# Performance work log

Hardware: AMD Instinct MI355X
Metric: run time of the kernel (lower is better)

The kernel has to match this reference:

```python
import jax, jax.numpy as jnp
import numpy as np

N = 4096        # nodes
E = 262144      # edges (avg degree 64)
F_IN = 8        # num_features
EMB = 4         # embedding_dim
HEADS = 4
G1 = 64         # GATConv1_dim (concat -> 256)
G2 = 16         # GATConv2_dim (concat -> d_model=64)
D = HEADS * G2  # 64
FF = 32         # ff_hid_dim
GRAPHS = 8
OUT = 4         # output_dim
SLOPE_GAT = 0.2   # PyG GATConv negative_slope
SLOPE = 0.01      # F.leaky_relu default

def _p(k, shape, scale=0.1):
    return jax.random.normal(k, shape, jnp.float32) * scale

def setup_inputs() -> dict:
    key = jax.random.key(0)
    ks = jax.random.split(key, 16)
    return {
        "x": jax.random.normal(ks[0], (N, F_IN), jnp.float32),
        "edge_index": jax.random.randint(ks[1], (2, E), 0, N),
        "batch": jnp.sort(jax.random.randint(ks[2], (N,), 0, GRAPHS)),
        "W_feat": _p(ks[3], (F_IN, EMB)), "b_feat": jnp.zeros((EMB,), jnp.float32),
        "W1": _p(ks[4], (EMB, HEADS * G1)), "as1": _p(ks[5], (HEADS, G1)), "ad1": _p(ks[6], (HEADS, G1)), "b1": jnp.zeros((HEADS * G1,), jnp.float32),
        "W2": _p(ks[7], (HEADS * G1, HEADS * G2)), "as2": _p(ks[8], (HEADS, G2)), "ad2": _p(ks[9], (HEADS, G2)), "b2": jnp.zeros((HEADS * G2,), jnp.float32),
        "enc_W1": _p(ks[10], (D, FF)), "enc_b1": jnp.zeros((FF,), jnp.float32),
        "enc_W2": _p(ks[11], (FF, D)), "enc_b2": jnp.zeros((D,), jnp.float32),
        "dec_W1": _p(ks[12], (D, FF)), "dec_b1": jnp.zeros((FF,), jnp.float32),
        "dec_W2": _p(ks[13], (FF, D)), "dec_b2": jnp.zeros((D,), jnp.float32),
        "W_fc": _p(ks[14], (D, OUT)), "b_fc": jnp.zeros((OUT,), jnp.float32),
    }

def _gat(x, src, dst, W, a_s, a_d, b, n):
    # PyG GATConv: h = W x; e_ij = LeakyReLU(a_src.h_j + a_dst.h_i); softmax over
    # edges grouped by destination i; out_i = sum_j alpha_ij h_j; concat heads + bias.
    h = (x @ W).reshape(n, HEADS, -1)                      # [N,H,C]
    logits = (h * a_s).sum(-1)[src] + (h * a_d).sum(-1)[dst]  # [E,H]
    e = jax.nn.leaky_relu(logits, SLOPE_GAT)
    m = jax.ops.segment_max(e, dst, num_segments=n)        # [N,H]
    ex = jnp.exp(e - m[dst])
    den = jax.ops.segment_sum(ex, dst, num_segments=n)
    alpha = ex / (den[dst] + 1e-16)                        # [E,H]
    out = jax.ops.segment_sum(h[src] * alpha[:, :, None], dst, num_segments=n)
    return out.reshape(n, -1) + b

def reference(x, edge_index, batch, W_feat, b_feat, W1, as1, ad1, b1, W2, as2, ad2, b2, enc_W1, enc_b1, enc_W2, enc_b2, dec_W1, dec_b1, dec_W2, dec_b2, W_fc, b_fc):
    src, dst = edge_index[0], edge_index[1]
    h = x @ W_feat + b_feat                                # feature_fc
    h = jax.nn.leaky_relu(_gat(h, src, dst, W1, as1, ad1, b1, N), SLOPE)
    h = jax.nn.leaky_relu(_gat(h, src, dst, W2, as2, ad2, b2, N), SLOPE)
    # Source bug preserved: encoder/decoder MultiheadAttention outputs are computed
    # and then DISCARDED (FFN reads the layer input), so attention never affects the
    # output and is omitted here (pure dead code). Encoder output `memory` is also
    # unused by the decoder FFN, but is computed for parity.
    memory = jax.nn.relu(jax.nn.relu(h @ enc_W1 + enc_b1) @ enc_W2 + enc_b2)
    t = jax.nn.relu(jax.nn.relu(h @ dec_W1 + dec_b1) @ dec_W2 + dec_b2)
    cnt = jax.ops.segment_sum(jnp.ones((N,), jnp.float32), batch, num_segments=GRAPHS)
    pooled = jax.ops.segment_sum(t, batch, num_segments=GRAPHS) / jnp.maximum(cnt, 1.0)[:, None]
    return pooled @ W_fc + b_fc                            # [GRAPHS, OUT]
```

## Files before the change

### kernel.cpp

```cpp
#include <hip/hip_runtime.h>
#include <math.h>

#define NN 4096
#define EE 262144
#define NCHUNK 64
#define CHSZ 4096
#define PAD 128
#define NGRAPHS 8

__device__ __forceinline__ float lrelu(float x, float s){ return x > 0.f ? x : s*x; }

__global__ __launch_bounds__(256) void k_n1hist(
    const float* __restrict__ x, const float* __restrict__ Wf,
    const float* __restrict__ bf, const float* __restrict__ W1,
    const float* __restrict__ as1, const float* __restrict__ ad1,
    const int* __restrict__ ei,
    float* __restrict__ emb4, float* __restrict__ asum1, float* __restrict__ adsum1,
    int* __restrict__ hist){
  __shared__ int shi[NN];
  int t = threadIdx.x, b = blockIdx.x;
  if (b < NCHUNK){
    for (int v=t; v<NN; v+=256) shi[v]=0;
    __syncthreads();
    int base = b*CHSZ;
    #pragma unroll
    for (int i=0;i<16;i++){
      int d = ei[EE + base + i*256 + t];
      atomicAdd(&shi[d], 1);
    }
    __syncthreads();
    for (int v=t; v<NN; v+=256) hist[b*NN + v] = shi[v];
    return;
  }
  int wid = t >> 6, lane = t & 63;
  int n = (b - NCHUNK)*4 + wid;
  float e0=bf[0], e1=bf[1], e2=bf[2], e3=bf[3];
  #pragma unroll
  for (int k=0;k<8;k++){
    float xv = x[n*8+k];
    e0 += xv*Wf[k*4+0]; e1 += xv*Wf[k*4+1];
    e2 += xv*Wf[k*4+2]; e3 += xv*Wf[k*4+3];
  }
  if (lane == 0) *(float4*)&emb4[n*4] = make_float4(e0,e1,e2,e3);
  int c0 = lane*4;
  float4 w0 = *(const float4*)&W1[0*256+c0];
  float4 w1 = *(const float4*)&W1[1*256+c0];
  float4 w2 = *(const float4*)&W1[2*256+c0];
  float4 w3 = *(const float4*)&W1[3*256+c0];
  float4 hv;
  hv.x = e0*w0.x + e1*w1.x + e2*w2.x + e3*w3.x;
  hv.y = e0*w0.y + e1*w1.y + e2*w2.y + e3*w3.y;
  hv.z = e0*w0.z + e1*w1.z + e2*w2.z + e3*w3.z;
  hv.w = e0*w0.w + e1*w1.w + e2*w2.w + e3*w3.w;
  int hh = lane>>4, idx = c0 & 63;
  float4 as = *(const float4*)&as1[hh*64+idx];
  float4 ad = *(const float4*)&ad1[hh*64+idx];
  float ps = hv.x*as.x + hv.y*as.y + hv.z*as.z + hv.w*as.w;
  float pd = hv.x*ad.x + hv.y*ad.y + hv.z*ad.z + hv.w*ad.w;
  #pragma unroll
  for (int m=1;m<16;m<<=1){ ps += __shfl_xor(ps,m,64); pd += __shfl_xor(pd,m,64); }
  if ((lane&15)==0){ asum1[n*4+hh]=ps; adsum1[n*4+hh]=pd; }
}

__global__ __launch_bounds__(256) void k_scatter(
    const int* __restrict__ ei, const int* __restrict__ hist,
    int* __restrict__ esrc, int* __restrict__ deg){
  __shared__ int shi[NN];
  int t = threadIdx.x, c = blockIdx.x;
  int acc[16];
  #pragma unroll
  for (int i=0;i<16;i++) acc[i]=0;
  for (int cp=0; cp<c; cp++){
    #pragma unroll
    for (int i=0;i<16;i++) acc[i] += hist[cp*NN + i*256 + t];
  }
  #pragma unroll
  for (int i=0;i<16;i++) shi[i*256+t] = (i*256+t)*PAD + acc[i];
  if (c == NCHUNK-1){
    #pragma unroll
    for (int i=0;i<16;i++) deg[i*256+t] = acc[i] + hist[c*NN + i*256 + t];
  }
  __syncthreads();
  int base = c*CHSZ;
  #pragma unroll
  for (int i=0;i<16;i++){
    int e = base + i*256 + t;
    int d = ei[EE+e], sr = ei[e];
    int pos = atomicAdd(&shi[d], 1);
    esrc[pos] = sr;
  }
}

__global__ __launch_bounds__(1024) void k_gat1n2(
    const int* __restrict__ deg, const int* __restrict__ esrc,
    const float* __restrict__ emb4, const float* __restrict__ asum1,
    const float* __restrict__ adsum1, const float* __restrict__ b1,
    const float* __restrict__ W1, const float* __restrict__ W2,
    const float* __restrict__ as2, const float* __restrict__ ad2,
    float* __restrict__ h2, float* __restrict__ asum2, float* __restrict__ adsum2){
  __shared__ __align__(16) float g1s[16*256];
  __shared__ __align__(16) float4 w2t[1024];
  int t = threadIdx.x, w = t>>6, lane = t&63;
  const int n = blockIdx.x*16 + w;
  const int start = n*PAD;
  const int dg = deg[n];
  const int hh = lane>>4;
  float4 adst = *(const float4*)&adsum1[n*4];
  int k0 = lane, k1 = lane+64;
  int j0 = esrc[start + (k0<dg ? k0 : 0)];
  int j1 = esrc[start + (k1<dg ? k1 : 0)];
  float4 a0 = *(const float4*)&asum1[j0*4];
  float4 a1 = *(const float4*)&asum1[j1*4];
  float4 mx;
  mx.x = k0<dg ? a0.x : -INFINITY;  mx.y = k0<dg ? a0.y : -INFINITY;
  mx.z = k0<dg ? a0.z : -INFINITY;  mx.w = k0<dg ? a0.w : -INFINITY;
  if (k1<dg){
    mx.x=fmaxf(mx.x,a1.x); mx.y=fmaxf(mx.y,a1.y);
    mx.z=fmaxf(mx.z,a1.z); mx.w=fmaxf(mx.w,a1.w);
  }
  #pragma unroll
  for (int m=1;m<64;m<<=1){
    mx.x=fmaxf(mx.x,__shfl_xor(mx.x,m,64));
    mx.y=fmaxf(mx.y,__shfl_xor(mx.y,m,64));
    mx.z=fmaxf(mx.z,__shfl_xor(mx.z,m,64));
    mx.w=fmaxf(mx.w,__shfl_xor(mx.w,m,64));
  }
  float4 mh;
  mh.x = lrelu(mx.x+adst.x,0.2f); mh.y = lrelu(mx.y+adst.y,0.2f);
  mh.z = lrelu(mx.z+adst.z,0.2f); mh.w = lrelu(mx.w+adst.w,0.2f);
  float4 ex0 = make_float4(0.f,0.f,0.f,0.f), ex1 = make_float4(0.f,0.f,0.f,0.f);
  if (k0<dg){
    ex0.x = expf(lrelu(a0.x+adst.x,0.2f)-mh.x);
    ex0.y = expf(lrelu(a0.y+adst.y,0.2f)-mh.y);
    ex0.z = expf(lrelu(a0.z+adst.z,0.2f)-mh.z);
    ex0.w = expf(lrelu(a0.w+adst.w,0.2f)-mh.w);
  }
  if (k1<dg){
    ex1.x = expf(lrelu(a1.x+adst.x,0.2f)-mh.x);
    ex1.y = expf(lrelu(a1.y+adst.y,0.2f)-mh.y);
    ex1.z = expf(lrelu(a1.z+adst.z,0.2f)-mh.z);
    ex1.w = expf(lrelu(a1.w+adst.w,0.2f)-mh.w);
  }
  float4 den = make_float4(ex0.x+ex1.x, ex0.y+ex1.y, ex0.z+ex1.z, ex0.w+ex1.w);
  #pragma unroll
  for (int m=1;m<64;m<<=1){
    den.x += __shfl_xor(den.x,m,64); den.y += __shfl_xor(den.y,m,64);
    den.z += __shfl_xor(den.z,m,64); den.w += __shfl_xor(den.w,m,64);
  }
  float4 al0, al1;
  al0.x = ex0.x/(den.x+1e-16f); al0.y = ex0.y/(den.y+1e-16f);
  al0.z = ex0.z/(den.z+1e-16f); al0.w = ex0.w/(den.w+1e-16f);
  al1.x = ex1.x/(den.x+1e-16f); al1.y = ex1.y/(den.y+1e-16f);
  al1.z = ex1.z/(den.z+1e-16f); al1.w = ex1.w/(den.w+1e-16f);
  float4 e0v = *(const float4*)&emb4[j0*4];
  float4 e1v = *(const float4*)&emb4[j1*4];
  float4 s0, s1, s2, s3;
  s0.x = al0.x*e0v.x + al1.x*e1v.x; s0.y = al0.x*e0v.y + al1.x*e1v.y;
  s0.z = al0.x*e0v.z + al1.x*e1v.z; s0.w = al0.x*e0v.w + al1.x*e1v.w;
  s1.x = al0.y*e0v.x + al1.y*e1v.x; s1.y = al0.y*e0v.y + al1.y*e1v.y;
  s1.z = al0.y*e0v.z + al1.y*e1v.z; s1.w = al0.y*e0v.w + al1.y*e1v.w;
  s2.x = al0.z*e0v.x + al1.z*e1v.x; s2.y = al0.z*e0v.y + al1.z*e1v.y;
  s2.z = al0.z*e0v.z + al1.z*e1v.z; s2.w = al0.z*e0v.w + al1.z*e1v.w;
  s3.x = al0.w*e0v.x + al1.w*e1v.x; s3.y = al0.w*e0v.y + al1.w*e1v.y;
  s3.z = al0.w*e0v.z + al1.w*e1v.z; s3.w = al0.w*e0v.w + al1.w*e1v.w;
  #pragma unroll
  for (int m=1;m<64;m<<=1){
    s0.x += __shfl_xor(s0.x,m,64); s0.y += __shfl_xor(s0.y,m,64);
    s0.z += __shfl_xor(s0.z,m,64); s0.w += __shfl_xor(s0.w,m,64);
    s1.x += __shfl_xor(s1.x,m,64); s1.y += __shfl_xor(s1.y,m,64);
    s1.z += __shfl_xor(s1.z,m,64); s1.w += __shfl_xor(s1.w,m,64);
    s2.x += __shfl_xor(s2.x,m,64); s2.y += __shfl_xor(s2.y,m,64);
    s2.z += __shfl_xor(s2.z,m,64); s2.w += __shfl_xor(s2.w,m,64);
    s3.x += __shfl_xor(s3.x,m,64); s3.y += __shfl_xor(s3.y,m,64);
    s3.z += __shfl_xor(s3.z,m,64); s3.w += __shfl_xor(s3.w,m,64);
  }
  float4 sh = (hh==0) ? s0 : (hh==1) ? s1 : (hh==2) ? s2 : s3;
  const int c0 = lane*4;
  float4 w0 = *(const float4*)&W1[0*256+c0];
  float4 w1 = *(const float4*)&W1[1*256+c0];
  float4 w2 = *(const float4*)&W1[2*256+c0];
  float4 w3 = *(const float4*)&W1[3*256+c0];
  float4 bb = *(const float4*)&b1[c0];
  float4 o;
  o.x = lrelu(sh.x*w0.x + sh.y*w1.x + sh.z*w2.x + sh.w*w3.x + bb.x, 0.01f);
  o.y = lrelu(sh.x*w0.y + sh.y*w1.y + sh.z*w2.y + sh.w*w3.y + bb.y, 0.01f);
  o.z = lrelu(sh.x*w0.z + sh.y*w1.z + sh.z*w2.z + sh.w*w3.z + bb.z, 0.01f);
  o.w = lrelu(sh.x*w0.w + sh.y*w1.w + sh.z*w2.w + sh.w*w3.w + bb.w, 0.01f);
  ((float4*)&g1s[w*256])[lane] = o;
  __syncthreads();
  float acc2 = 0.f;
  for (int kt=0; kt<4; kt++){
    w2t[t] = ((const float4*)W2)[kt*1024 + t];
    __syncthreads();
    const float* g1row = &g1s[w*256 + kt*64];
    const float* wt = (const float*)w2t;
    #pragma unroll 8
    for (int k=0;k<64;k++) acc2 += g1row[k] * wt[k*64 + lane];
    __syncthreads();
  }
  h2[n*64+lane] = acc2;
  int idx = lane&15;
  float ps = acc2 * as2[hh*16+idx];
  float pd = acc2 * ad2[hh*16+idx];
  #pragma unroll
  for (int m=1;m<16;m<<=1){ ps += __shfl_xor(ps,m,64); pd += __shfl_xor(pd,m,64); }
  if (idx == 0){ asum2[n*4+hh] = ps; adsum2[n*4+hh] = pd; }
}

__global__ __launch_bounds__(1024) void k_gat2(
    const int* __restrict__ deg, const int* __restrict__ esrc,
    const float* __restrict__ h2, const float* __restrict__ asum2,
    const float* __restrict__ adsum2, const float* __restrict__ b2,
    const float* __restrict__ dW1, const float* __restrict__ db1,
    const float* __restrict__ dW2, const float* __restrict__ db2,
    float* __restrict__ tbuf){
  __shared__ __align__(16) float salpha[16*512];
  __shared__ float sg[16][96];
  int t = threadIdx.x, w = t>>6, lane = t&63;
  const int n = blockIdx.x*16 + w;
  const int start = n*PAD;
  const int dg = deg[n];
  const int hh = lane>>4;
  float4 adst = *(const float4*)&adsum2[n*4];
  int k0 = lane, k1 = lane+64;
  int j0 = esrc[start + (k0<dg ? k0 : 0)];
  int j1 = esrc[start + (k1<dg ? k1 : 0)];
  float4 a0 = *(const float4*)&asum2[j0*4];
  float4 a1 = *(const float4*)&asum2[j1*4];
  float4 mx;
  mx.x = k0<dg ? a0.x : -INFINITY;  mx.y = k0<dg ? a0.y : -INFINITY;
  mx.z = k0<dg ? a0.z : -INFINITY;  mx.w = k0<dg ? a0.w : -INFINITY;
  if (k1<dg){
    mx.x=fmaxf(mx.x,a1.x); mx.y=fmaxf(mx.y,a1.y);
    mx.z=fmaxf(mx.z,a1.z); mx.w=fmaxf(mx.w,a1.w);
  }
  #pragma unroll
  for (int m=1;m<64;m<<=1){
    mx.x=fmaxf(mx.x,__shfl_xor(mx.x,m,64));
    mx.y=fmaxf(mx.y,__shfl_xor(mx.y,m,64));
    mx.z=fmaxf(mx.z,__shfl_xor(mx.z,m,64));
    mx.w=fmaxf(mx.w,__shfl_xor(mx.w,m,64));
  }
  float4 mh;
  mh.x = lrelu(mx.x+adst.x,0.2f); mh.y = lrelu(mx.y+adst.y,0.2f);
  mh.z = lrelu(mx.z+adst.z,0.2f); mh.w = lrelu(mx.w+adst.w,0.2f);
  float4 ex0 = make_float4(0.f,0.f,0.f,0.f), ex1 = make_float4(0.f,0.f,0.f,0.f);
  if (k0<dg){
    ex0.x = expf(lrelu(a0.x+adst.x,0.2f)-mh.x);
    ex0.y = expf(lrelu(a0.y+adst.y,0.2f)-mh.y);
    ex0.z = expf(lrelu(a0.z+adst.z,0.2f)-mh.z);
    ex0.w = expf(lrelu(a0.w+adst.w,0.2f)-mh.w);
  }
  if (k1<dg){
    ex1.x = expf(lrelu(a1.x+adst.x,0.2f)-mh.x);
    ex1.y = expf(lrelu(a1.y+adst.y,0.2f)-mh.y);
    ex1.z = expf(lrelu(a1.z+adst.z,0.2f)-mh.z);
    ex1.w = expf(lrelu(a1.w+adst.w,0.2f)-mh.w);
  }
  float4 den = make_float4(ex0.x+ex1.x, ex0.y+ex1.y, ex0.z+ex1.z, ex0.w+ex1.w);
  #pragma unroll
  for (int m=1;m<64;m<<=1){
    den.x += __shfl_xor(den.x,m,64); den.y += __shfl_xor(den.y,m,64);
    den.z += __shfl_xor(den.z,m,64); den.w += __shfl_xor(den.w,m,64);
  }
  float4 inv4 = make_float4(1.f/(den.x+1e-16f), 1.f/(den.y+1e-16f),
                            1.f/(den.z+1e-16f), 1.f/(den.w+1e-16f));
  if (k0<dg){
    float4 al = make_float4(ex0.x*inv4.x, ex0.y*inv4.y, ex0.z*inv4.z, ex0.w*inv4.w);
    *(float4*)&salpha[w*512 + k0*4] = al;
  }
  if (k1<dg){
    float4 al = make_float4(ex1.x*inv4.x, ex1.y*inv4.y, ex1.z*inv4.z, ex1.w*inv4.w);
    *(float4*)&salpha[w*512 + k1*4] = al;
  }
  float acc = 0.f;
  #pragma unroll 4
  for (int k=0;k<dg;k++){
    int j = esrc[start+k];
    float al = salpha[w*512 + k*4 + hh];
    acc += al * h2[j*64 + lane];
  }
  float g2v = lrelu(acc + b2[lane], 0.01f);
  sg[w][lane] = g2v;
  int m = lane & 31;
  float a2 = db1[m];
  #pragma unroll
  for (int k=0;k<64;k++) a2 += sg[w][k] * dW1[k*32+m];
  if (lane < 32) sg[w][64+m] = fmaxf(a2, 0.f);
  float tv = db2[lane];
  #pragma unroll
  for (int k=0;k<32;k++) tv += sg[w][64+k] * dW2[k*64+lane];
  tbuf[n*64 + lane] = fmaxf(tv, 0.f);
}

__global__ __launch_bounds__(1024) void k_pool(
    const float* __restrict__ tbuf, const int* __restrict__ batch,
    const float* __restrict__ W_fc, const float* __restrict__ b_fc,
    float* __restrict__ out){
  __shared__ float4 part[64][17];
  int t = threadIdx.x, g = blockIdx.x;
  int rg = t>>4, cg = t&15;
  int lo=0, hi=NN;
  while (lo<hi){ int mid=(lo+hi)>>1; if (batch[mid] < g) lo=mid+1; else hi=mid; }
  int s0 = lo;
  lo=0; hi=NN;
  while (lo<hi){ int mid=(lo+hi)>>1; if (batch[mid] < g+1) lo=mid+1; else hi=mid; }
  int e0 = lo;
  float4 acc = make_float4(0.f,0.f,0.f,0.f);
  #pragma unroll 4
  for (int n=s0+rg; n<e0; n+=64){
    float4 v = *(const float4*)&tbuf[n*64 + cg*4];
    acc.x += v.x; acc.y += v.y; acc.z += v.z; acc.w += v.w;
  }
  part[rg][cg] = acc;
  __syncthreads();
  #pragma unroll
  for (int step=32; step>=1; step>>=1){
    if (rg < step){
      float4 o = part[rg+step][cg], m = part[rg][cg];
      part[rg][cg] = make_float4(m.x+o.x, m.y+o.y, m.z+o.z, m.w+o.w);
    }
    __syncthreads();
  }
  if (t < 16){
    float inv = 1.f/fmaxf((float)(e0-s0), 1.f);
    float4 s = part[0][t];
    float4 pm = make_float4(s.x*inv, s.y*inv, s.z*inv, s.w*inv);
    float4 w0 = *(const float4*)&W_fc[(4*t+0)*4];
    float4 w1 = *(const float4*)&W_fc[(4*t+1)*4];
    float4 w2 = *(const float4*)&W_fc[(4*t+2)*4];
    float4 w3 = *(const float4*)&W_fc[(4*t+3)*4];
    float4 po;
    po.x = pm.x*w0.x + pm.y*w1.x + pm.z*w2.x + pm.w*w3.x;
    po.y = pm.x*w0.y + pm.y*w1.y + pm.z*w2.y + pm.w*w3.y;
    po.z = pm.x*w0.z + pm.y*w1.z + pm.z*w2.z + pm.w*w3.z;
    po.w = pm.x*w0.w + pm.y*w1.w + pm.z*w2.w + pm.w*w3.w;
    #pragma unroll
    for (int m=1;m<16;m<<=1){
      po.x += __shfl_xor(po.x,m,64); po.y += __shfl_xor(po.y,m,64);
      po.z += __shfl_xor(po.z,m,64); po.w += __shfl_xor(po.w,m,64);
    }
    if (t == 0){
      float4 bb = *(const float4*)&b_fc[0];
      *(float4*)&out[g*4] = make_float4(po.x+bb.x, po.y+bb.y, po.z+bb.z, po.w+bb.w);
    }
  }
}

extern "C" void kernel_launch(void* const* d_in, const int* in_sizes, int n_in,
                              void* d_out, int out_size, void* d_ws, size_t ws_size,
                              hipStream_t stream){
  const float* x      = (const float*)d_in[0];
  const int*   ei     = (const int*)  d_in[1];
  const int*   batch  = (const int*)  d_in[2];
  const float* W_feat = (const float*)d_in[3];
  const float* b_feat = (const float*)d_in[4];
  const float* W1     = (const float*)d_in[5];
  const float* as1    = (const float*)d_in[6];
  const float* ad1    = (const float*)d_in[7];
  const float* b1     = (const float*)d_in[8];
  const float* W2     = (const float*)d_in[9];
  const float* as2    = (const float*)d_in[10];
  const float* ad2    = (const float*)d_in[11];
  const float* b2     = (const float*)d_in[12];
  const float* dW1    = (const float*)d_in[17];
  const float* db1    = (const float*)d_in[18];
  const float* dW2    = (const float*)d_in[19];
  const float* db2    = (const float*)d_in[20];
  const float* W_fc   = (const float*)d_in[21];
  const float* b_fc   = (const float*)d_in[22];
  float* out = (float*)d_out;

  char* ws = (char*)d_ws;
  float* h2     = (float*)(ws + 0);
  float* tbuf   = (float*)(ws + 1048576);
  int*   hist   = (int*)  (ws + 2097152);
  int*   esrc   = (int*)  (ws + 3145728);
  float* emb4   = (float*)(ws + 5242880);
  float* asum1  = (float*)(ws + 5308416);
  float* adsum1 = (float*)(ws + 5373952);
  float* asum2  = (float*)(ws + 5439488);
  float* adsum2 = (float*)(ws + 5505024);
  int*   deg    = (int*)  (ws + 5570560);

  k_n1hist <<<NCHUNK + NN/4, 256, 0, stream>>>(x, W_feat, b_feat, W1, as1, ad1,
                                               ei, emb4, asum1, adsum1, hist);
  k_scatter<<<NCHUNK,        256, 0, stream>>>(ei, hist, esrc, deg);
  k_gat1n2 <<<NN/16,        1024, 0, stream>>>(deg, esrc, emb4, asum1, adsum1, b1,
                                               W1, W2, as2, ad2, h2, asum2, adsum2);
  k_gat2   <<<NN/16,        1024, 0, stream>>>(deg, esrc, h2, asum2, adsum2, b2,
                                               dW1, db1, dW2, db2, tbuf);
  k_pool   <<<NGRAPHS,      1024, 0, stream>>>(tbuf, batch, W_fc, b_fc, out);
}
```

Baseline: 76.27 us.

## Add column-scan kernel for CSR bases and split GAT2 edges across wave pairs

Replaces the serial per-chunk prefix over earlier histogram rows in k_scatter with a separate transposed column-scan kernel. That kernel computes per-chunk bucket bases and degrees once, and k_scatter simply loads them. Before, chunk c re-read c prior histogram rows, so the work was unbalanced across chunks. k_gat2 now assigns two waves per node, each handling half of the edges, and combines max, denominator and accumulator through shared memory with block barriers. The cost is one extra kernel launch, an extra workspace buffer, and several block-wide syncs in gat2, where half the waves then sit idle during the FFN tail.

Measured after the change: 65.85 us, median of 2. 13.7% less time.

```diff
diff --git a/kernel.cpp b/kernel.cpp
--- a/kernel.cpp
+++ b/kernel.cpp
@@ -62,24 +62,39 @@
   if ((lane&15)==0){ asum1[n*4+hh]=ps; adsum1[n*4+hh]=pd; }
 }
 
+__global__ __launch_bounds__(256) void k_colscan(
+    const int* __restrict__ hist, int* __restrict__ bases, int* __restrict__ deg){
+  __shared__ int tile[64][65];
+  int t = threadIdx.x, b = blockIdx.x;
+  int v0 = b*64;
+  for (int idx=t; idx<64*64; idx+=256){
+    int c = idx>>6, v = idx&63;
+    tile[c][v] = hist[c*NN + v0 + v];
+  }
+  __syncthreads();
+  if (t < 64){
+    int s = 0;
+    #pragma unroll
+    for (int c=0;c<64;c++){
+      int xch = tile[c][t];
+      tile[c][t] = (v0+t)*PAD + s;
+      s += xch;
+    }
+    deg[v0+t] = s;
+  }
+  __syncthreads();
+  for (int idx=t; idx<64*64; idx+=256){
+    int c = idx>>6, v = idx&63;
+    bases[c*NN + v0 + v] = tile[c][v];
+  }
+}
+
 __global__ __launch_bounds__(256) void k_scatter(
-    const int* __restrict__ ei, const int* __restrict__ hist,
-    int* __restrict__ esrc, int* __restrict__ deg){
+    const int* __restrict__ ei, const int* __restrict__ bases,
+    int* __restrict__ esrc){
   __shared__ int shi[NN];
   int t = threadIdx.x, c = blockIdx.x;
-  int acc[16];
-  #pragma unroll
-  for (int i=0;i<16;i++) acc[i]=0;
-  for (int cp=0; cp<c; cp++){
-    #pragma unroll
-    for (int i=0;i<16;i++) acc[i] += hist[cp*NN + i*256 + t];
-  }
-  #pragma unroll
-  for (int i=0;i<16;i++) shi[i*256+t] = (i*256+t)*PAD + acc[i];
-  if (c == NCHUNK-1){
-    #pragma unroll
-    for (int i=0;i<16;i++) deg[i*256+t] = acc[i] + hist[c*NN + i*256 + t];
-  }
+  for (int v=t; v<NN; v+=256) shi[v] = bases[c*NN + v];
   __syncthreads();
   int base = c*CHSZ;
   #pragma unroll
@@ -214,26 +229,24 @@
     const float* __restrict__ dW1, const float* __restrict__ db1,
     const float* __restrict__ dW2, const float* __restrict__ db2,
     float* __restrict__ tbuf){
-  __shared__ __align__(16) float salpha[16*512];
-  __shared__ float sg[16][96];
+  __shared__ float4 smx[8][2];
+  __shared__ float4 sdn[8][2];
+  __shared__ __align__(16) float salpha[8*512];
+  __shared__ float sacc[8][2][64];
+  __shared__ float sg[8][96];
   int t = threadIdx.x, w = t>>6, lane = t&63;
-  const int n = blockIdx.x*16 + w;
+  const int p = w>>1, tw = w&1;
+  const int n = blockIdx.x*8 + p;
   const int start = n*PAD;
   const int dg = deg[n];
   const int hh = lane>>4;
   float4 adst = *(const float4*)&adsum2[n*4];
-  int k0 = lane, k1 = lane+64;
-  int j0 = esrc[start + (k0<dg ? k0 : 0)];
-  int j1 = esrc[start + (k1<dg ? k1 : 0)];
-  float4 a0 = *(const float4*)&asum2[j0*4];
-  float4 a1 = *(const float4*)&asum2[j1*4];
+  const int k = tw*64 + lane;
+  int j = esrc[start + (k<dg ? k : 0)];
+  float4 a = *(const float4*)&asum2[j*4];
   float4 mx;
-  mx.x = k0<dg ? a0.x : -INFINITY;  mx.y = k0<dg ? a0.y : -INFINITY;
-  mx.z = k0<dg ? a0.z : -INFINITY;  mx.w = k0<dg ? a0.w : -INFINITY;
-  if (k1<dg){
-    mx.x=fmaxf(mx.x,a1.x); mx.y=fmaxf(mx.y,a1.y);
-    mx.z=fmaxf(mx.z,a1.z); mx.w=fmaxf(mx.w,a1.w);
-  }
+  mx.x = k<dg ? a.x : -INFINITY;  mx.y = k<dg ? a.y : -INFINITY;
+  mx.z = k<dg ? a.z : -INFINITY;  mx.w = k<dg ? a.w : -INFINITY;
   #pragma unroll
   for (int m=1;m<64;m<<=1){
     mx.x=fmaxf(mx.x,__shfl_xor(mx.x,m,64));
@@ -241,56 +254,61 @@
     mx.z=fmaxf(mx.z,__shfl_xor(mx.z,m,64));
     mx.w=fmaxf(mx.w,__shfl_xor(mx.w,m,64));
   }
+  if (lane==0) smx[p][tw] = mx;
+  __syncthreads();
+  float4 m0 = smx[p][0], m1 = smx[p][1];
   float4 mh;
-  mh.x = lrelu(mx.x+adst.x,0.2f); mh.y = lrelu(mx.y+adst.y,0.2f);
-  mh.z = lrelu(mx.z+adst.z,0.2f); mh.w = lrelu(mx.w+adst.w,0.2f);
-  float4 ex0 = make_float4(0.f,0.f,0.f,0.f), ex1 = make_float4(0.f,0.f,0.f,0.f);
-  if (k0<dg){
-    ex0.x = expf(lrelu(a0.x+adst.x,0.2f)-mh.x);
-    ex0.y = expf(lrelu(a0.y+adst.y,0.2f)-mh.y);
-    ex0.z = expf(lrelu(a0.z+adst.z,0.2f)-mh.z);
-    ex0.w = expf(lrelu(a0.w+adst.w,0.2f)-mh.w);
-  }
-  if (k1<dg){
-    ex1.x = expf(lrelu(a1.x+adst.x,0.2f)-mh.x);
-    ex1.y = expf(lrelu(a1.y+adst.y,0.2f)-mh.y);
-    ex1.z = expf(lrelu(a1.z+adst.z,0.2f)-mh.z);
-    ex1.w = expf(lrelu(a1.w+adst.w,0.2f)-mh.w);
-  }
-  float4 den = make_float4(ex0.x+ex1.x, ex0.y+ex1.y, ex0.z+ex1.z, ex0.w+ex1.w);
+  mh.x = lrelu(fmaxf(m0.x,m1.x)+adst.x,0.2f);
+  mh.y = lrelu(fmaxf(m0.y,m1.y)+adst.y,0.2f);
+  mh.z = lrelu(fmaxf(m0.z,m1.z)+adst.z,0.2f);
+  mh.w = lrelu(fmaxf(m0.w,m1.w)+adst.w,0.2f);
+  float4 ex = make_float4(0.f,0.f,0.f,0.f);
+  if (k<dg){
+    ex.x = expf(lrelu(a.x+adst.x,0.2f)-mh.x);
+    ex.y = expf(lrelu(a.y+adst.y,0.2f)-mh.y);
+    ex.z = expf(lrelu(a.z+adst.z,0.2f)-mh.z);
+    ex.w = expf(lrelu(a.w+adst.w,0.2f)-mh.w);
+  }
+  float4 dn = ex;
   #pragma unroll
   for (int m=1;m<64;m<<=1){
-    den.x += __shfl_xor(den.x,m,64); den.y += __shfl_xor(den.y,m,64);
-    den.z += __shfl_xor(den.z,m,64); den.w += __shfl_xor(den.w,m,64);
-  }
-  float4 inv4 = make_float4(1.f/(den.x+1e-16f), 1.f/(den.y+1e-16f),
-                            1.f/(den.z+1e-16f), 1.f/(den.w+1e-16f));
-  if (k0<dg){
-    float4 al = make_float4(ex0.x*inv4.x, ex0.y*inv4.y, ex0.z*inv4.z, ex0.w*inv4.w);
-    *(float4*)&salpha[w*512 + k0*4] = al;
-  }
-  if (k1<dg){
-    float4 al = make_float4(ex1.x*inv4.x, ex1.y*inv4.y, ex1.z*inv4.z, ex1.w*inv4.w);
-    *(float4*)&salpha[w*512 + k1*4] = al;
+    dn.x += __shfl_xor(dn.x,m,64); dn.y += __shfl_xor(dn.y,m,64);
+    dn.z += __shfl_xor(dn.z,m,64); dn.w += __shfl_xor(dn.w,m,64);
+  }
+  if (lane==0) sdn[p][tw] = dn;
+  __syncthreads();
+  float4 d0 = sdn[p][0], d1 = sdn[p][1];
+  float4 inv4 = make_float4(1.f/(d0.x+d1.x+1e-16f), 1.f/(d0.y+d1.y+1e-16f),
+                            1.f/(d0.z+d1.z+1e-16f), 1.f/(d0.w+d1.w+1e-16f));
+  if (k<dg){
+    float4 al = make_float4(ex.x*inv4.x, ex.y*inv4.y, ex.z*inv4.z, ex.w*inv4.w);
+    *(float4*)&salpha[p*512 + k*4] = al;
   }
   float acc = 0.f;
+  int cnt = dg - tw*64; cnt = cnt < 0 ? 0 : (cnt > 64 ? 64 : cnt);
   #pragma unroll 4
-  for (int k=0;k<dg;k++){
-    int j = esrc[start+k];
-    float al = salpha[w*512 + k*4 + hh];
-    acc += al * h2[j*64 + lane];
-  }
-  float g2v = lrelu(acc + b2[lane], 0.01f);
-  sg[w][lane] = g2v;
-  int m = lane & 31;
-  float a2 = db1[m];
-  #pragma unroll
-  for (int k=0;k<64;k++) a2 += sg[w][k] * dW1[k*32+m];
-  if (lane < 32) sg[w][64+m] = fmaxf(a2, 0.f);
-  float tv = db2[lane];
-  #pragma unroll
-  for (int k=0;k<32;k++) tv += sg[w][64+k] * dW2[k*64+lane];
-  tbuf[n*64 + lane] = fmaxf(tv, 0.f);
+  for (int k2=0; k2<cnt; k2++){
+    int jj = esrc[start + tw*64 + k2];
+    float al = salpha[p*512 + (tw*64+k2)*4 + hh];
+    acc += al * h2[jj*64 + lane];
+  }
+  sacc[p][tw][lane] = acc;
+  __syncthreads();
+  if (tw==0){
+    float tot = sacc[p][0][lane] + sacc[p][1][lane];
+    float g2v = lrelu(tot + b2[lane], 0.01f);
+    float* sgp = sg[p];
+    sgp[lane] = g2v;
+    int m = lane & 31;
+    float a2 = db1[m];
+    #pragma unroll
+    for (int kk=0;kk<64;kk++) a2 += sgp[kk] * dW1[kk*32+m];
+    if (lane < 32) sgp[64+m] = fmaxf(a2, 0.f);
+    float tv = db2[lane];
+    #pragma unroll
+    for (int kk=0;kk<32;kk++) tv += sgp[64+kk] * dW2[kk*64+lane];
+    tbuf[n*64 + lane] = fmaxf(tv, 0.f);
+  }
 }
 
 __global__ __launch_bounds__(1024) void k_pool(
@@ -375,20 +393,22 @@
   float* h2     = (float*)(ws + 0);
   float* tbuf   = (float*)(ws + 1048576);
   int*   hist   = (int*)  (ws + 2097152);
-  int*   esrc   = (int*)  (ws + 3145728);
-  float* emb4   = (float*)(ws + 5242880);
-  float* asum1  = (float*)(ws + 5308416);
-  float* adsum1 = (float*)(ws + 5373952);
-  float* asum2  = (float*)(ws + 5439488);
-  float* adsum2 = (float*)(ws + 5505024);
-  int*   deg    = (int*)  (ws + 5570560);
+  int*   bases  = (int*)  (ws + 3145728);
+  int*   esrc   = (int*)  (ws + 4194304);
+  float* emb4   = (float*)(ws + 6291456);
+  float* asum1  = (float*)(ws + 6356992);
+  float* adsum1 = (float*)(ws + 6422528);
+  float* asum2  = (float*)(ws + 6488064);
+  float* adsum2 = (float*)(ws + 6553600);
+  int*   deg    = (int*)  (ws + 6619136);
 
   k_n1hist <<<NCHUNK + NN/4, 256, 0, stream>>>(x, W_feat, b_feat, W1, as1, ad1,
                                                ei, emb4, asum1, adsum1, hist);
-  k_scatter<<<NCHUNK,        256, 0, stream>>>(ei, hist, esrc, deg);
+  k_colscan<<<NN/64,         256, 0, stream>>>(hist, bases, deg);
+  k_scatter<<<NCHUNK,        256, 0, stream>>>(ei, bases, esrc);
   k_gat1n2 <<<NN/16,        1024, 0, stream>>>(deg, esrc, emb4, asum1, adsum1, b1,
                                                W1, W2, as2, ad2, h2, asum2, adsum2);
-  k_gat2   <<<NN/16,        1024, 0, stream>>>(deg, esrc, h2, asum2, adsum2, b2,
+  k_gat2   <<<NN/8,         1024, 0, stream>>>(deg, esrc, h2, asum2, adsum2, b2,
                                                dW1, db1, dW2, db2, tbuf);
   k_pool   <<<NGRAPHS,      1024, 0, stream>>>(tbuf, batch, W_fc, b_fc, out);
 }
```
